# Performance work log

Measured on AMD Instinct MI355X. Metric: run time of the kernel, lower is better.

## Reference

```python
import jax, jax.numpy as jnp
import numpy as np

TEMPERATURE = 0.1


def setup_inputs() -> dict:
    key = jax.random.key(0)
    # Scale by 0.03 so exp((z/T)@(z/T).T) stays finite in fp32 (module uses
    # an unstabilized exp-sum-log, and the diagonal is ||z||^2 / T^2).
    z = jax.random.normal(key, (16384, 128), dtype=jnp.float32) * 0.03
    return {"z": z}


def reference(z) -> jnp.ndarray:
    n = z.shape[0]
    zs = z / TEMPERATURE                      # [N, d]
    a = zs @ zs.T                             # [N, N] self-similarity
    # Faithful to the original: -log(sum(exp(a), axis=1) / N), then mean.
    l = -jnp.log(jnp.exp(a).sum(axis=1) / n)  # [N]
    return l.mean()
```

## Files before the change

kernel.cpp:

```cpp
#include <hip/hip_runtime.h>
#include <stdint.h>

#define NROW 16384
#define DDIM 128
#define ROWB 256

constexpr int NB     = 64;
constexpr int NJT    = NROW / NB;
constexpr int CHUNK  = 8;
constexpr int NSTRIP = 128;
constexpr int NBLK   = 2112;

typedef __bf16 bf16x8 __attribute__((ext_vector_type(8)));
typedef float  f32x4  __attribute__((ext_vector_type(4)));
typedef int    i32x4  __attribute__((ext_vector_type(4)));

typedef const uint32_t __attribute__((address_space(1)))* gptr_t;
typedef uint32_t __attribute__((address_space(3)))*       lptr_t;

__device__ __forceinline__ unsigned short f2bf(float x) {
  union { float f; uint32_t u; } c; c.f = x;
  uint32_t u = c.u + 0x7fffu + ((c.u >> 16) & 1u);
  return (unsigned short)(u >> 16);
}

__device__ __forceinline__ int Sfun(int k) {
  const int q = k >> 2, r = k & 3;
  return 2 * q * (q + 1) + r * (q + 1);
}

__global__ __launch_bounds__(256) void prep_kernel(const float* __restrict__ z,
                                                   unsigned short* __restrict__ zs,
                                                   float* __restrict__ s) {
  const float SC = 12.011224087864498f;
  int t = blockIdx.x * 256 + threadIdx.x;
  float4 v = reinterpret_cast<const float4*>(z)[t];
  ushort4 o;
  o.x = f2bf(v.x * SC); o.y = f2bf(v.y * SC);
  o.z = f2bf(v.z * SC); o.w = f2bf(v.w * SC);
  reinterpret_cast<ushort4*>(zs)[t] = o;
  if (t < NROW) s[t] = 0.0f;
}

__global__ __launch_bounds__(256, 2) void gemm_exp_kernel(const unsigned short* __restrict__ zs,
                                                          float* __restrict__ s) {
  __shared__ __align__(16) char smem[2 * NB * ROWB + 4 * CHUNK * 64 * 4];
  float* csm = (float*)(smem + 2 * NB * ROWB);
  const int tid  = threadIdx.x;
  const int lane = tid & 63;
  const int wid  = tid >> 6;

  int I, c;
  {
    const int bid = blockIdx.x;
    const int m = NBLK - bid;
    int k = (int)sqrtf(8.0f * (float)m);
    if (k > 128) k = 128;
    if (k < 1) k = 1;
    while (Sfun(k) < m) ++k;
    while (k > 1 && Sfun(k - 1) >= m) --k;
    I = 128 - k;
    c = bid - (NBLK - Sfun(k));
  }
  const int mI     = NJT - 2 * I;
  const int jt0    = 2 * I + CHUNK * c;
  const int JT_blk = min(CHUNK, mI - CHUNK * c);

  const int rowBase = I * 128 + wid * 32;
  const char* zb = (const char*)zs;
  const int kb = (lane >> 4) << 4;

  bf16x8 afrag[2][4];
  {
    const int r0 = rowBase + (lane & 15);
#pragma unroll
    for (int mf = 0; mf < 2; ++mf)
#pragma unroll
      for (int ks = 0; ks < 4; ++ks) {
        i32x4 raw = *reinterpret_cast<const i32x4*>(
            zb + (size_t)(r0 + mf * 16) * ROWB + ks * 64 + kb);
        afrag[mf][ks] = __builtin_bit_cast(bf16x8, raw);
      }
  }

  f32x4 rsv[2];
  float cs[4];
  rsv[0] = (f32x4){0.f, 0.f, 0.f, 0.f};
  rsv[1] = (f32x4){0.f, 0.f, 0.f, 0.f};
#pragma unroll
  for (int nf = 0; nf < 4; ++nf) cs[nf] = 0.0f;

#define STAGE_B(buf, k)                                                          \
  {                                                                              \
    _Pragma("unroll")                                                            \
    for (int i_ = 0; i_ < 4; ++i_) {                                             \
      const int destByte_ = wid * 4096 + i_ * 1024 + lane * 16;                  \
      const int r_  = destByte_ >> 8;                                            \
      const int cb_ = destByte_ & 0xF0;                                          \
      const int srcByte_ = ((jt0 + (k)) * NB + r_) * ROWB                        \
                           + (cb_ ^ ((r_ & 15) << 4));                           \
      __builtin_amdgcn_global_load_lds((gptr_t)(zb + srcByte_),                  \
          (lptr_t)(smem + (buf) * (NB * ROWB) + destByte_), 16, 0, 0);           \
    }                                                                            \
  }

  STAGE_B(0, 0);

#pragma unroll 1
  for (int k = 0; k < JT_blk; ++k) {
    const int cur = k & 1;
    if (k + 1 < JT_blk) {
      STAGE_B(cur ^ 1, k + 1);
      asm volatile("s_waitcnt vmcnt(4)" ::: "memory");
    } else {
      asm volatile("s_waitcnt vmcnt(0)" ::: "memory");
    }
    __builtin_amdgcn_s_barrier();

    f32x4 acc[2][4];
#pragma unroll
    for (int mf = 0; mf < 2; ++mf)
#pragma unroll
      for (int nf = 0; nf < 4; ++nf) {
        f32x4 zv = {0.f, 0.f, 0.f, 0.f};
        acc[mf][nf] = zv;
      }

    __builtin_amdgcn_s_setprio(1);
    const char* bufp = smem + cur * (NB * ROWB);
#pragma unroll
    for (int ks = 0; ks < 4; ++ks) {
      bf16x8 bfrag[4];
#pragma unroll
      for (int nf = 0; nf < 4; ++nf) {
        const int r   = nf * 16 + (lane & 15);
        const int kk  = ks * 64 + kb;
        const int off = r * ROWB + (kk ^ ((r & 15) << 4));
        i32x4 raw = *reinterpret_cast<const i32x4*>(bufp + off);
        bfrag[nf] = __builtin_bit_cast(bf16x8, raw);
      }
#pragma unroll
      for (int mf = 0; mf < 2; ++mf)
#pragma unroll
        for (int nf = 0; nf < 4; ++nf)
          acc[mf][nf] = __builtin_amdgcn_mfma_f32_16x16x32_bf16(
              afrag[mf][ks], bfrag[nf], acc[mf][nf], 0, 0, 0);
    }
    __builtin_amdgcn_s_setprio(0);

#pragma unroll
    for (int mf = 0; mf < 2; ++mf)
#pragma unroll
      for (int nf = 0; nf < 4; ++nf) {
        f32x4 a4 = acc[mf][nf];
        f32x4 ev;
        ev[0] = __builtin_amdgcn_exp2f(a4[0]);
        ev[1] = __builtin_amdgcn_exp2f(a4[1]);
        ev[2] = __builtin_amdgcn_exp2f(a4[2]);
        ev[3] = __builtin_amdgcn_exp2f(a4[3]);
        rsv[mf] += ev;
        cs[nf] += (ev[0] + ev[1]) + (ev[2] + ev[3]);
      }

#pragma unroll
    for (int nf = 0; nf < 4; ++nf) {
      float v = cs[nf];
      v += __shfl_xor(v, 16);
      v += __shfl_xor(v, 32);
      if (lane < 16) csm[wid * (CHUNK * 64) + k * 64 + nf * 16 + lane] = v;
      cs[nf] = 0.0f;
    }

    __builtin_amdgcn_s_barrier();
  }
#undef STAGE_B

#pragma unroll
  for (int mf = 0; mf < 2; ++mf)
#pragma unroll
    for (int r = 0; r < 4; ++r) {
      float v = rsv[mf][r];
      v += __shfl_xor(v, 1);
      v += __shfl_xor(v, 2);
      v += __shfl_xor(v, 4);
      v += __shfl_xor(v, 8);
      if ((lane & 15) == 0) {
        const int row = rowBase + mf * 16 + ((lane >> 4) << 2) + r;
        atomicAdd(&s[row], v);
      }
    }

  __syncthreads();
  {
    const int colBase0 = jt0 * NB;
    const int diagEnd  = (I + 1) * 128;
    const int ncol     = JT_blk * NB;
#pragma unroll
    for (int k4 = 0; k4 < 2; ++k4) {
      const int idx = k4 * 256 + tid;
      if (idx < ncol) {
        const int col = colBase0 + idx;
        if (col >= diagEnd) {
          float sum = csm[idx] + csm[CHUNK * 64 + idx]
                    + csm[2 * CHUNK * 64 + idx] + csm[3 * CHUNK * 64 + idx];
          atomicAdd(&s[col], sum);
        }
      }
    }
  }
}

__global__ __launch_bounds__(1024) void reduce_kernel(const float* __restrict__ s,
                                                      float* __restrict__ out) {
  const int tid = threadIdx.x;
  float acc = 0.0f;
  for (int i = tid; i < NROW; i += 1024) acc += __log2f(s[i]);
#pragma unroll
  for (int m = 32; m >= 1; m >>= 1) acc += __shfl_xor(acc, m);
  __shared__ float wsum[16];
  if ((tid & 63) == 0) wsum[tid >> 6] = acc;
  __syncthreads();
  if (tid == 0) {
    float tot = 0.0f;
#pragma unroll
    for (int w = 0; w < 16; ++w) tot += wsum[w];
    out[0] = logf((float)NROW) - 0.6931471805599453f * tot / (float)NROW;
  }
}

extern "C" void kernel_launch(void* const* d_in, const int* in_sizes, int n_in,
                              void* d_out, int out_size, void* d_ws, size_t ws_size,
                              hipStream_t stream) {
  const float* z = (const float*)d_in[0];
  unsigned short* zs = (unsigned short*)d_ws;
  float* s = (float*)((char*)d_ws + (size_t)NROW * DDIM * 2);
  float* out = (float*)d_out;

  prep_kernel<<<dim3(NROW * DDIM / 4 / 256), dim3(256), 0, stream>>>(z, zs, s);
  gemm_exp_kernel<<<dim3(NBLK), dim3(256), 0, stream>>>(zs, s);
  reduce_kernel<<<dim3(1), dim3(1024), 0, stream>>>(s, out);
}
```

Baseline: 65.34 us.

## Unroll GEMM loop by two with precomputed staging offsets and parallelize final reduction

Unrolls the main GEMM/exp loop by two over fixed double-buffer offsets, precomputing LDS read pointers and global staging offsets so per-iteration address arithmetic disappears. The first B tile is issued before the A fragments load, and the first MFMA seeds from a zero constant instead of zeroing accumulators. The single-block log reduction becomes a 64-block kernel that atomically adds scaled partial sums into an output preinitialized with log(N) in prep. This cuts scalar overhead and the serial tail, at the cost of float atomics that make the result order-dependent.

```diff
diff --git a/kernel.cpp b/kernel.cpp
--- a/kernel.cpp
+++ b/kernel.cpp
@@ -8,7 +8,6 @@
 constexpr int NB     = 64;
 constexpr int NJT    = NROW / NB;
 constexpr int CHUNK  = 8;
-constexpr int NSTRIP = 128;
 constexpr int NBLK   = 2112;
 
 typedef __bf16 bf16x8 __attribute__((ext_vector_type(8)));
@@ -31,7 +30,8 @@
 
 __global__ __launch_bounds__(256) void prep_kernel(const float* __restrict__ z,
                                                    unsigned short* __restrict__ zs,
-                                                   float* __restrict__ s) {
+                                                   float* __restrict__ s,
+                                                   float* __restrict__ out) {
   const float SC = 12.011224087864498f;
   int t = blockIdx.x * 256 + threadIdx.x;
   float4 v = reinterpret_cast<const float4*>(z)[t];
@@ -40,6 +40,7 @@
   o.z = f2bf(v.z * SC); o.w = f2bf(v.w * SC);
   reinterpret_cast<ushort4*>(zs)[t] = o;
   if (t < NROW) s[t] = 0.0f;
+  if (t == 0) out[0] = 9.704060527839234f;
 }
 
 __global__ __launch_bounds__(256, 2) void gemm_exp_kernel(const unsigned short* __restrict__ zs,
@@ -70,6 +71,35 @@
   const char* zb = (const char*)zs;
   const int kb = (lane >> 4) << 4;
 
+  const char* rq[4];
+  {
+    const int r = lane & 15;
+#pragma unroll
+    for (int ks = 0; ks < 4; ++ks)
+      rq[ks] = smem + r * 256 + ((ks * 64 + kb) ^ (r << 4));
+  }
+  const int dBase = wid * 4096 + lane * 16;
+  int sOff[4];
+#pragma unroll
+  for (int i_ = 0; i_ < 4; ++i_) {
+    const int db  = dBase + i_ * 1024;
+    const int r_  = db >> 8;
+    const int cb_ = db & 0xF0;
+    sOff[i_] = (jt0 * NB + r_) * ROWB + (cb_ ^ ((r_ & 15) << 4));
+  }
+
+#define STAGE(P)                                                               \
+  {                                                                            \
+    _Pragma("unroll")                                                          \
+    for (int i_ = 0; i_ < 4; ++i_) {                                           \
+      __builtin_amdgcn_global_load_lds((gptr_t)(zb + sOff[i_]),                \
+          (lptr_t)(smem + (P) + dBase + i_ * 1024), 16, 0, 0);                 \
+      sOff[i_] += NB * ROWB;                                                   \
+    }                                                                          \
+  }
+
+  STAGE(0);
+
   bf16x8 afrag[2][4];
   {
     const int r0 = rowBase + (lane & 15);
@@ -89,91 +119,86 @@
   rsv[1] = (f32x4){0.f, 0.f, 0.f, 0.f};
 #pragma unroll
   for (int nf = 0; nf < 4; ++nf) cs[nf] = 0.0f;
-
-#define STAGE_B(buf, k)                                                          \
-  {                                                                              \
-    _Pragma("unroll")                                                            \
-    for (int i_ = 0; i_ < 4; ++i_) {                                             \
-      const int destByte_ = wid * 4096 + i_ * 1024 + lane * 16;                  \
-      const int r_  = destByte_ >> 8;                                            \
-      const int cb_ = destByte_ & 0xF0;                                          \
-      const int srcByte_ = ((jt0 + (k)) * NB + r_) * ROWB                        \
-                           + (cb_ ^ ((r_ & 15) << 4));                           \
-      __builtin_amdgcn_global_load_lds((gptr_t)(zb + srcByte_),                  \
-          (lptr_t)(smem + (buf) * (NB * ROWB) + destByte_), 16, 0, 0);           \
-    }                                                                            \
-  }
-
-  STAGE_B(0, 0);
-
+  const f32x4 kZ = {0.f, 0.f, 0.f, 0.f};
+
+#define COMPUTE(P, kk)                                                         \
+  {                                                                            \
+    f32x4 acc[2][4];                                                           \
+    __builtin_amdgcn_s_setprio(1);                                             \
+    _Pragma("unroll")                                                          \
+    for (int ks = 0; ks < 4; ++ks) {                                           \
+      bf16x8 bfr[4];                                                           \
+      _Pragma("unroll")                                                        \
+      for (int nf = 0; nf < 4; ++nf)                                           \
+        bfr[nf] = __builtin_bit_cast(bf16x8,                                   \
+            *reinterpret_cast<const i32x4*>(rq[ks] + nf * 4096 + (P)));        \
+      if (ks == 0) {                                                           \
+        _Pragma("unroll")                                                      \
+        for (int mf = 0; mf < 2; ++mf)                                         \
+          _Pragma("unroll")                                                    \
+          for (int nf = 0; nf < 4; ++nf)                                       \
+            acc[mf][nf] = __builtin_amdgcn_mfma_f32_16x16x32_bf16(             \
+                afrag[mf][0], bfr[nf], kZ, 0, 0, 0);                           \
+      } else {                                                                 \
+        _Pragma("unroll")                                                      \
+        for (int mf = 0; mf < 2; ++mf)                                         \
+          _Pragma("unroll")                                                    \
+          for (int nf = 0; nf < 4; ++nf)                                       \
+            acc[mf][nf] = __builtin_amdgcn_mfma_f32_16x16x32_bf16(             \
+                afrag[mf][ks], bfr[nf], acc[mf][nf], 0, 0, 0);                 \
+      }                                                                        \
+    }                                                                          \
+    __builtin_amdgcn_s_setprio(0);                                             \
+    _Pragma("unroll")                                                          \
+    for (int mf = 0; mf < 2; ++mf)                                             \
+      _Pragma("unroll")                                                        \
+      for (int nf = 0; nf < 4; ++nf) {                                         \
+        f32x4 a4 = acc[mf][nf];                                                \
+        f32x4 ev;                                                              \
+        ev[0] = __builtin_amdgcn_exp2f(a4[0]);                                 \
+        ev[1] = __builtin_amdgcn_exp2f(a4[1]);                                 \
+        ev[2] = __builtin_amdgcn_exp2f(a4[2]);                                 \
+        ev[3] = __builtin_amdgcn_exp2f(a4[3]);                                 \
+        rsv[mf] += ev;                                                         \
+        cs[nf] += (ev[0] + ev[1]) + (ev[2] + ev[3]);                           \
+      }                                                                        \
+    _Pragma("unroll")                                                          \
+    for (int nf = 0; nf < 4; ++nf) {                                           \
+      float v = cs[nf];                                                        \
+      v += __shfl_xor(v, 16);                                                  \
+      v += __shfl_xor(v, 32);                                                  \
+      if (lane < 16) csm[wid * (CHUNK * 64) + (kk) * 64 + nf * 16 + lane] = v; \
+      cs[nf] = 0.0f;                                                           \
+    }                                                                          \
+  }
+
+  int k = 0;
 #pragma unroll 1
-  for (int k = 0; k < JT_blk; ++k) {
-    const int cur = k & 1;
-    if (k + 1 < JT_blk) {
-      STAGE_B(cur ^ 1, k + 1);
+  for (; k + 2 <= JT_blk; k += 2) {
+    STAGE(16384);
+    asm volatile("s_waitcnt vmcnt(4)" ::: "memory");
+    __builtin_amdgcn_s_barrier();
+    COMPUTE(0, k);
+    __builtin_amdgcn_s_barrier();
+
+    if (k + 2 < JT_blk) {
+      STAGE(0);
       asm volatile("s_waitcnt vmcnt(4)" ::: "memory");
     } else {
       asm volatile("s_waitcnt vmcnt(0)" ::: "memory");
     }
     __builtin_amdgcn_s_barrier();
-
-    f32x4 acc[2][4];
-#pragma unroll
-    for (int mf = 0; mf < 2; ++mf)
-#pragma unroll
-      for (int nf = 0; nf < 4; ++nf) {
-        f32x4 zv = {0.f, 0.f, 0.f, 0.f};
-        acc[mf][nf] = zv;
-      }
-
-    __builtin_amdgcn_s_setprio(1);
-    const char* bufp = smem + cur * (NB * ROWB);
-#pragma unroll
-    for (int ks = 0; ks < 4; ++ks) {
-      bf16x8 bfrag[4];
-#pragma unroll
-      for (int nf = 0; nf < 4; ++nf) {
-        const int r   = nf * 16 + (lane & 15);
-        const int kk  = ks * 64 + kb;
-        const int off = r * ROWB + (kk ^ ((r & 15) << 4));
-        i32x4 raw = *reinterpret_cast<const i32x4*>(bufp + off);
-        bfrag[nf] = __builtin_bit_cast(bf16x8, raw);
-      }
-#pragma unroll
-      for (int mf = 0; mf < 2; ++mf)
-#pragma unroll
-        for (int nf = 0; nf < 4; ++nf)
-          acc[mf][nf] = __builtin_amdgcn_mfma_f32_16x16x32_bf16(
-              afrag[mf][ks], bfrag[nf], acc[mf][nf], 0, 0, 0);
-    }
-    __builtin_amdgcn_s_setprio(0);
-
-#pragma unroll
-    for (int mf = 0; mf < 2; ++mf)
-#pragma unroll
-      for (int nf = 0; nf < 4; ++nf) {
-        f32x4 a4 = acc[mf][nf];
-        f32x4 ev;
-        ev[0] = __builtin_amdgcn_exp2f(a4[0]);
-        ev[1] = __builtin_amdgcn_exp2f(a4[1]);
-        ev[2] = __builtin_amdgcn_exp2f(a4[2]);
-        ev[3] = __builtin_amdgcn_exp2f(a4[3]);
-        rsv[mf] += ev;
-        cs[nf] += (ev[0] + ev[1]) + (ev[2] + ev[3]);
-      }
-
-#pragma unroll
-    for (int nf = 0; nf < 4; ++nf) {
-      float v = cs[nf];
-      v += __shfl_xor(v, 16);
-      v += __shfl_xor(v, 32);
-      if (lane < 16) csm[wid * (CHUNK * 64) + k * 64 + nf * 16 + lane] = v;
-      cs[nf] = 0.0f;
-    }
-
-    __builtin_amdgcn_s_barrier();
-  }
-#undef STAGE_B
+    COMPUTE(16384, k + 1);
+    __builtin_amdgcn_s_barrier();
+  }
+  if (k < JT_blk) {
+    asm volatile("s_waitcnt vmcnt(0)" ::: "memory");
+    __builtin_amdgcn_s_barrier();
+    COMPUTE(0, k);
+    __builtin_amdgcn_s_barrier();
+  }
+#undef STAGE
+#undef COMPUTE
 
 #pragma unroll
   for (int mf = 0; mf < 2; ++mf)
@@ -210,21 +235,20 @@
   }
 }
 
-__global__ __launch_bounds__(1024) void reduce_kernel(const float* __restrict__ s,
-                                                      float* __restrict__ out) {
-  const int tid = threadIdx.x;
-  float acc = 0.0f;
-  for (int i = tid; i < NROW; i += 1024) acc += __log2f(s[i]);
-#pragma unroll
-  for (int m = 32; m >= 1; m >>= 1) acc += __shfl_xor(acc, m);
-  __shared__ float wsum[16];
-  if ((tid & 63) == 0) wsum[tid >> 6] = acc;
+__global__ __launch_bounds__(256) void reduce_kernel(const float* __restrict__ s,
+                                                     float* __restrict__ out) {
+  const int tid  = threadIdx.x;
+  const int lane = tid & 63;
+  const int wid  = tid >> 6;
+  float v = __log2f(s[blockIdx.x * 256 + tid]);
+#pragma unroll
+  for (int m = 32; m >= 1; m >>= 1) v += __shfl_xor(v, m);
+  __shared__ float ws[4];
+  if (lane == 0) ws[wid] = v;
   __syncthreads();
   if (tid == 0) {
-    float tot = 0.0f;
-#pragma unroll
-    for (int w = 0; w < 16; ++w) tot += wsum[w];
-    out[0] = logf((float)NROW) - 0.6931471805599453f * tot / (float)NROW;
+    const float t = ws[0] + ws[1] + ws[2] + ws[3];
+    atomicAdd(out, -4.2307473367321867e-5f * t);
   }
 }
 
@@ -236,7 +260,7 @@
   float* s = (float*)((char*)d_ws + (size_t)NROW * DDIM * 2);
   float* out = (float*)d_out;
 
-  prep_kernel<<<dim3(NROW * DDIM / 4 / 256), dim3(256), 0, stream>>>(z, zs, s);
+  prep_kernel<<<dim3(NROW * DDIM / 4 / 256), dim3(256), 0, stream>>>(z, zs, s, out);
   gemm_exp_kernel<<<dim3(NBLK), dim3(256), 0, stream>>>(zs, s);
-  reduce_kernel<<<dim3(1), dim3(1024), 0, stream>>>(s, out);
-}
+  reduce_kernel<<<dim3(64), dim3(256), 0, stream>>>(s, out);
+}
```

Result: no change. 64.90 us (-0.7%).
